# Kernel tuning notes

Measured on AMD Instinct MI355X. Metric: run time of the kernel, lower is better.

The kernel has to match this reference:

```python
import jax, jax.numpy as jnp
import numpy as np

B, H, S, D = 4, 16, 2048, 64

def setup_inputs() -> dict:
    key = jax.random.key(0)
    kq, kk, kv = jax.random.split(key, 3)
    return {
        "input_query": jax.random.normal(kq, (B, H, S, D), dtype=jnp.float32),
        "input_key": jax.random.normal(kk, (B, H, S, D), dtype=jnp.float32),
        "input_value": jax.random.normal(kv, (B, H, S, D), dtype=jnp.float32),
    }

def reference(input_query, input_key, input_value):
    # Unscaled, unmasked attention: softmax(Q K^T) V
    scores = jnp.einsum("bhsd,bhtd->bhst", input_query, input_key)  # [B,H,S,S]
    probs = jax.nn.softmax(scores, axis=-1)
    return jnp.einsum("bhst,bhtd->bhsd", probs, input_value)  # [B,H,S,D]
```

## Files before the change

### kernel.cpp

```cpp
#include <hip/hip_runtime.h>
#include <hip/hip_bf16.h>
#include <stdint.h>

#define SEQ 2048
#define DIM 64
#define NH  64
#define KT  32
#define NT  (SEQ / KT)
#define RAWK_BYTES 8192
#define FRAG_BYTES 12288
#define KF_BYTES   8192

typedef __attribute__((ext_vector_type(8)))  short    bf16x8;
typedef __attribute__((ext_vector_type(8)))  _Float16 f16x8;
typedef __attribute__((ext_vector_type(8)))  float    f32x8;
typedef __attribute__((ext_vector_type(16))) float    f32x16;
typedef unsigned int u32;

#if __has_builtin(__builtin_amdgcn_exp2f)
#define EXP2(x) __builtin_amdgcn_exp2f(x)
#else
#define EXP2(x) exp2f(x)
#endif

__device__ __forceinline__ int phi(int s) {
    int h = (s >> 2) & 1, b = s >> 3, i = s & 3;
    return 8 * h + 4 * b + i + (b >= 2 ? 8 : 0);
}

__global__ __launch_bounds__(768, 6) void attn_fused(
    const float* __restrict__ Q, const float* __restrict__ K,
    const float* __restrict__ V, float* __restrict__ O)
{
    __shared__ __align__(16) char rawK[3][RAWK_BYTES];
    __shared__ __align__(16) char frag[3][FRAG_BYTES];

    const int tid  = threadIdx.x;
    const int wave = tid >> 6, lane = tid & 63;
    const int h = lane >> 5, col = lane & 31;

    const int bid  = blockIdx.x;
    const int head = (bid & 7) * 8 + ((bid >> 3) & 7);
    const size_t base = (size_t)head * SEQ * DIM;

    if (wave < 8) {
        const int qw = (bid >> 6) * 256 + wave * 32;

        f16x8 qf[4];
        {
            const float* qr = Q + base + (size_t)(qw + col) * DIM;
            #pragma unroll
            for (int c = 0; c < 4; ++c)
                #pragma unroll
                for (int j = 0; j < 8; ++j)
                    qf[c][j] = (_Float16)(qr[c * 16 + 8 * h + j] * 1.44269504088896f);
        }

        f32x16 z16;
        #pragma unroll
        for (int r = 0; r < 16; ++r) z16[r] = 0.f;
        f32x16 of[2];
        of[0] = z16; of[1] = z16;
        float l_own = 0.f;

        __builtin_amdgcn_s_barrier();

        int fi = 0;
        for (int kt = 0; kt < NT; ++kt) {
            asm volatile("s_waitcnt lgkmcnt(0)" ::: "memory");
            __builtin_amdgcn_s_barrier();
            __builtin_amdgcn_sched_barrier(0);
            const char* cur = frag[fi];

            f32x16 s = z16;
            __builtin_amdgcn_s_setprio(1);
            #pragma unroll
            for (int c = 0; c < 4; ++c) {
                f16x8 kh = *(const f16x8*)(cur + (c * 2 + 0) * 1024 + lane * 16);
                f16x8 kl = *(const f16x8*)(cur + (c * 2 + 1) * 1024 + lane * 16);
                s = __builtin_amdgcn_mfma_f32_32x32x16_f16(kh, qf[c], s, 0, 0, 0);
                s = __builtin_amdgcn_mfma_f32_32x32x16_f16(kl, qf[c], s, 0, 0, 0);
            }
            __builtin_amdgcn_s_setprio(0);

            bf16x8 pfrag[2];
            {
                float p[16], ls = 0.f;
                #pragma unroll
                for (int r = 0; r < 16; ++r) { p[r] = EXP2(s[r]); ls += p[r]; }
                l_own += ls;
                u32 pk[8];
                #pragma unroll
                for (int m = 0; m < 8; ++m) {
                    __hip_bfloat162 b2 = __float22bfloat162_rn(make_float2(p[2 * m], p[2 * m + 1]));
                    __builtin_memcpy(&pk[m], &b2, 4);
                }
                #pragma unroll
                for (int c = 0; c < 2; ++c) {
                    u32 a0 = pk[4 * c + 0], b0 = pk[4 * c + 2];
                    u32 a1 = pk[4 * c + 1], b1 = pk[4 * c + 3];
                    asm volatile("v_permlane32_swap_b32 %0, %1" : "+v"(a0), "+v"(b0));
                    asm volatile("v_permlane32_swap_b32 %0, %1" : "+v"(a1), "+v"(b1));
                    union { u32 w[4]; bf16x8 v; } fr;
                    fr.w[0] = a0; fr.w[1] = a1; fr.w[2] = b0; fr.w[3] = b1;
                    pfrag[c] = fr.v;
                }
            }

            __builtin_amdgcn_s_setprio(1);
            #pragma unroll
            for (int f = 0; f < 2; ++f)
                #pragma unroll
                for (int c = 0; c < 2; ++c) {
                    bf16x8 vf = *(const bf16x8*)(cur + KF_BYTES + (f * 2 + c) * 1024 + lane * 16);
                    of[f] = __builtin_amdgcn_mfma_f32_32x32x16_bf16(pfrag[c], vf, of[f], 0, 0, 0);
                }
            __builtin_amdgcn_s_setprio(0);

            fi = (fi == 2) ? 0 : fi + 1;
        }

        float* op = O + base;
        {
            float lall = l_own + __shfl_xor(l_own, 32);
            float inv = 1.0f / lall;
            #pragma unroll
            for (int r = 0; r < 16; ++r) {
                int qrow = (r & 3) + 8 * (r >> 2) + 4 * h;
                float iq = __shfl(inv, qrow);
                op[(size_t)(qw + qrow) * DIM + col]      = of[0][r] * iq;
                op[(size_t)(qw + qrow) * DIM + 32 + col] = of[1][r] * iq;
            }
        }
    } else {
        const int pw = wave - 8;
        const float* Kh = K + base;
        const float* Vh = V + base;

        const int fv = pw >> 1, cv = pw & 1;
        int vrow[8];
        #pragma unroll
        for (int j = 0; j < 8; ++j) vrow[j] = phi(16 * cv + 8 * h + j);

        auto stageK = [&](int kt, char* dst) {
            const char* g = (const char*)(Kh + (size_t)kt * (KT * DIM));
            #pragma unroll
            for (int i = 0; i < 2; ++i) {
                const int P  = pw * 128 + i * 64 + lane;
                const int sk = (P & ~15) | ((P & 15) ^ ((P >> 4) & 7));
                char* d = dst + (size_t)(pw * 128 + i * 64) * 16;
                __builtin_amdgcn_global_load_lds(
                    (const __attribute__((address_space(1))) u32*)(g + (size_t)sk * 16),
                    (__attribute__((address_space(3))) u32*)d, 16, 0, 0);
            }
        };
        auto loadV = [&](int kt) -> f32x8 {
            const float* vp = Vh + (size_t)kt * (KT * DIM) + fv * 32 + col;
            f32x8 r;
            #pragma unroll
            for (int j = 0; j < 8; ++j) r[j] = vp[vrow[j] * DIM];
            return r;
        };
        auto convert = [&](const char* rk_, char* fr, f32x8 vv) {
            const int r = phi(col);
            const int kk = 4 * pw + 2 * h;
            const float4* rk4 = (const float4*)rk_;
            float4 a = rk4[r * 16 + ((kk    ) ^ (r & 7))];
            float4 b = rk4[r * 16 + ((kk + 1) ^ (r & 7))];
            float x[8] = {a.x, a.y, a.z, a.w, b.x, b.y, b.z, b.w};
            f16x8 hi, lo;
            #pragma unroll
            for (int j = 0; j < 8; ++j) {
                _Float16 xh = (_Float16)x[j];
                hi[j] = xh;
                lo[j] = (_Float16)(x[j] - (float)xh);
            }
            *(f16x8*)(fr + (pw * 2 + 0) * 1024 + lane * 16) = hi;
            *(f16x8*)(fr + (pw * 2 + 1) * 1024 + lane * 16) = lo;
            union { u32 w[4]; bf16x8 v; } uv;
            #pragma unroll
            for (int j = 0; j < 4; ++j) {
                __hip_bfloat162 b2 = __float22bfloat162_rn(make_float2(vv[2 * j], vv[2 * j + 1]));
                __builtin_memcpy(&uv.w[j], &b2, 4);
            }
            *(bf16x8*)(fr + KF_BYTES + (fv * 2 + cv) * 1024 + lane * 16) = uv.v;
        };

        stageK(0, rawK[0]);
        stageK(1, rawK[1]);
        f32x8 vvA = loadV(0);
        f32x8 vvB = loadV(1);
        asm volatile("s_waitcnt vmcnt(0)" ::: "memory");
        __builtin_amdgcn_s_barrier();
        convert(rawK[0], frag[0], vvA);
        convert(rawK[1], frag[1], vvB);
        stageK(2, rawK[2]);
        vvA = loadV(2);

        int ri = 2, si = 0;
        for (int kt = 0; kt < NT; ++kt) {
            asm volatile("s_waitcnt vmcnt(0) lgkmcnt(0)" ::: "memory");
            __builtin_amdgcn_s_barrier();
            __builtin_amdgcn_sched_barrier(0);

            const bool ld = (kt + 3 < NT);
            if (ld) stageK(kt + 3, rawK[si]);
            f32x8 vnext;
            if (ld) vnext = loadV(kt + 3);
            if (kt + 2 < NT)
                convert(rawK[ri], frag[ri], (kt & 1) ? vvB : vvA);
            if (ld) { if (kt & 1) vvA = vnext; else vvB = vnext; }

            ri = (ri == 2) ? 0 : ri + 1;
            si = (si == 2) ? 0 : si + 1;
        }
    }
}

extern "C" void kernel_launch(void* const* d_in, const int* in_sizes, int n_in,
                              void* d_out, int out_size, void* d_ws, size_t ws_size,
                              hipStream_t stream) {
    const float* Q = (const float*)d_in[0];
    const float* K = (const float*)d_in[1];
    const float* V = (const float*)d_in[2];
    float* Out = (float*)d_out;
    (void)d_ws; (void)ws_size;

    attn_fused<<<dim3(NH * (SEQ / 256)), dim3(768), 0, stream>>>(Q, K, V, Out);
}
```

Before: 229.3 us.

## Process two query tiles per consumer wave and halve block size

Each compute wave now handles 64 query rows (two 32-row tiles) instead of 32. This reuses every K/V fragment read from LDS across two MFMA chains, and halves the number of consumer and producer waves per block (384 threads instead of 768). Producer waves each stage twice as much K and V per tile. The change raises register pressure per wave and lowers the wave count per block, which trades latency hiding for less LDS traffic and fewer barrier participants.

```diff
diff --git a/kernel.cpp b/kernel.cpp
--- a/kernel.cpp
+++ b/kernel.cpp
@@ -28,7 +28,7 @@
     return 8 * h + 4 * b + i + (b >= 2 ? 8 : 0);
 }
 
-__global__ __launch_bounds__(768, 6) void attn_fused(
+__global__ __launch_bounds__(384, 3) void attn_fused(
     const float* __restrict__ Q, const float* __restrict__ K,
     const float* __restrict__ V, float* __restrict__ O)
 {
@@ -43,25 +43,26 @@
     const int head = (bid & 7) * 8 + ((bid >> 3) & 7);
     const size_t base = (size_t)head * SEQ * DIM;
 
-    if (wave < 8) {
-        const int qw = (bid >> 6) * 256 + wave * 32;
-
-        f16x8 qf[4];
-        {
-            const float* qr = Q + base + (size_t)(qw + col) * DIM;
+    if (wave < 4) {
+        const int qw = (bid >> 6) * 256 + wave * 64;
+
+        f16x8 qf[2][4];
+        #pragma unroll
+        for (int qt = 0; qt < 2; ++qt) {
+            const float* qr = Q + base + (size_t)(qw + qt * 32 + col) * DIM;
             #pragma unroll
             for (int c = 0; c < 4; ++c)
                 #pragma unroll
                 for (int j = 0; j < 8; ++j)
-                    qf[c][j] = (_Float16)(qr[c * 16 + 8 * h + j] * 1.44269504088896f);
+                    qf[qt][c][j] = (_Float16)(qr[c * 16 + 8 * h + j] * 1.44269504088896f);
         }
 
         f32x16 z16;
         #pragma unroll
         for (int r = 0; r < 16; ++r) z16[r] = 0.f;
-        f32x16 of[2];
-        of[0] = z16; of[1] = z16;
-        float l_own = 0.f;
+        f32x16 of[2][2];
+        of[0][0] = z16; of[0][1] = z16; of[1][0] = z16; of[1][1] = z16;
+        float l_own[2] = {0.f, 0.f};
 
         __builtin_amdgcn_s_barrier();
 
@@ -72,23 +73,30 @@
             __builtin_amdgcn_sched_barrier(0);
             const char* cur = frag[fi];
 
-            f32x16 s = z16;
+            f32x16 s[2]; s[0] = z16; s[1] = z16;
             __builtin_amdgcn_s_setprio(1);
             #pragma unroll
             for (int c = 0; c < 4; ++c) {
                 f16x8 kh = *(const f16x8*)(cur + (c * 2 + 0) * 1024 + lane * 16);
                 f16x8 kl = *(const f16x8*)(cur + (c * 2 + 1) * 1024 + lane * 16);
-                s = __builtin_amdgcn_mfma_f32_32x32x16_f16(kh, qf[c], s, 0, 0, 0);
-                s = __builtin_amdgcn_mfma_f32_32x32x16_f16(kl, qf[c], s, 0, 0, 0);
+                s[0] = __builtin_amdgcn_mfma_f32_32x32x16_f16(kh, qf[0][c], s[0], 0, 0, 0);
+                s[0] = __builtin_amdgcn_mfma_f32_32x32x16_f16(kl, qf[0][c], s[0], 0, 0, 0);
+                s[1] = __builtin_amdgcn_mfma_f32_32x32x16_f16(kh, qf[1][c], s[1], 0, 0, 0);
+                s[1] = __builtin_amdgcn_mfma_f32_32x32x16_f16(kl, qf[1][c], s[1], 0, 0, 0);
             }
             __builtin_amdgcn_s_setprio(0);
 
-            bf16x8 pfrag[2];
-            {
-                float p[16], ls = 0.f;
-                #pragma unroll
-                for (int r = 0; r < 16; ++r) { p[r] = EXP2(s[r]); ls += p[r]; }
-                l_own += ls;
+            bf16x8 pfrag[2][2];
+            #pragma unroll
+            for (int qt = 0; qt < 2; ++qt) {
+                float p[16];
+                #pragma unroll
+                for (int r = 0; r < 16; ++r) p[r] = EXP2(s[qt][r]);
+                float t0 = (p[0] + p[1]) + (p[2] + p[3]);
+                float t1 = (p[4] + p[5]) + (p[6] + p[7]);
+                float t2 = (p[8] + p[9]) + (p[10] + p[11]);
+                float t3 = (p[12] + p[13]) + (p[14] + p[15]);
+                l_own[qt] += (t0 + t1) + (t2 + t3);
                 u32 pk[8];
                 #pragma unroll
                 for (int m = 0; m < 8; ++m) {
@@ -103,7 +111,7 @@
                     asm volatile("v_permlane32_swap_b32 %0, %1" : "+v"(a1), "+v"(b1));
                     union { u32 w[4]; bf16x8 v; } fr;
                     fr.w[0] = a0; fr.w[1] = a1; fr.w[2] = b0; fr.w[3] = b1;
-                    pfrag[c] = fr.v;
+                    pfrag[qt][c] = fr.v;
                 }
             }
 
@@ -113,7 +121,8 @@
                 #pragma unroll
                 for (int c = 0; c < 2; ++c) {
                     bf16x8 vf = *(const bf16x8*)(cur + KF_BYTES + (f * 2 + c) * 1024 + lane * 16);
-                    of[f] = __builtin_amdgcn_mfma_f32_32x32x16_bf16(pfrag[c], vf, of[f], 0, 0, 0);
+                    of[0][f] = __builtin_amdgcn_mfma_f32_32x32x16_bf16(pfrag[0][c], vf, of[0][f], 0, 0, 0);
+                    of[1][f] = __builtin_amdgcn_mfma_f32_32x32x16_bf16(pfrag[1][c], vf, of[1][f], 0, 0, 0);
                 }
             __builtin_amdgcn_s_setprio(0);
 
@@ -121,81 +130,90 @@
         }
 
         float* op = O + base;
-        {
-            float lall = l_own + __shfl_xor(l_own, 32);
+        #pragma unroll
+        for (int qt = 0; qt < 2; ++qt) {
+            float lall = l_own[qt] + __shfl_xor(l_own[qt], 32);
             float inv = 1.0f / lall;
             #pragma unroll
             for (int r = 0; r < 16; ++r) {
                 int qrow = (r & 3) + 8 * (r >> 2) + 4 * h;
                 float iq = __shfl(inv, qrow);
-                op[(size_t)(qw + qrow) * DIM + col]      = of[0][r] * iq;
-                op[(size_t)(qw + qrow) * DIM + 32 + col] = of[1][r] * iq;
+                op[(size_t)(qw + qt * 32 + qrow) * DIM + col]      = of[qt][0][r] * iq;
+                op[(size_t)(qw + qt * 32 + qrow) * DIM + 32 + col] = of[qt][1][r] * iq;
             }
         }
     } else {
-        const int pw = wave - 8;
+        const int pw = wave - 4;
         const float* Kh = K + base;
         const float* Vh = V + base;
 
-        const int fv = pw >> 1, cv = pw & 1;
-        int vrow[8];
-        #pragma unroll
-        for (int j = 0; j < 8; ++j) vrow[j] = phi(16 * cv + 8 * h + j);
+        const int fv = pw;
+        int vrA[8], vrB[8];
+        #pragma unroll
+        for (int j = 0; j < 8; ++j) { vrA[j] = phi(8 * h + j); vrB[j] = phi(16 + 8 * h + j); }
 
         auto stageK = [&](int kt, char* dst) {
             const char* g = (const char*)(Kh + (size_t)kt * (KT * DIM));
             #pragma unroll
-            for (int i = 0; i < 2; ++i) {
-                const int P  = pw * 128 + i * 64 + lane;
+            for (int i = 0; i < 4; ++i) {
+                const int P  = pw * 256 + i * 64 + lane;
                 const int sk = (P & ~15) | ((P & 15) ^ ((P >> 4) & 7));
-                char* d = dst + (size_t)(pw * 128 + i * 64) * 16;
+                char* d = dst + (size_t)(pw * 256 + i * 64) * 16;
                 __builtin_amdgcn_global_load_lds(
                     (const __attribute__((address_space(1))) u32*)(g + (size_t)sk * 16),
                     (__attribute__((address_space(3))) u32*)d, 16, 0, 0);
             }
         };
-        auto loadV = [&](int kt) -> f32x8 {
+        auto loadV = [&](int kt, f32x8& ra, f32x8& rb) {
             const float* vp = Vh + (size_t)kt * (KT * DIM) + fv * 32 + col;
-            f32x8 r;
-            #pragma unroll
-            for (int j = 0; j < 8; ++j) r[j] = vp[vrow[j] * DIM];
-            return r;
+            #pragma unroll
+            for (int j = 0; j < 8; ++j) ra[j] = vp[vrA[j] * DIM];
+            #pragma unroll
+            for (int j = 0; j < 8; ++j) rb[j] = vp[vrB[j] * DIM];
         };
-        auto convert = [&](const char* rk_, char* fr, f32x8 vv) {
+        auto convert = [&](const char* rk_, char* fr, f32x8 va, f32x8 vb) {
+            const float4* rk4 = (const float4*)rk_;
             const int r = phi(col);
-            const int kk = 4 * pw + 2 * h;
-            const float4* rk4 = (const float4*)rk_;
-            float4 a = rk4[r * 16 + ((kk    ) ^ (r & 7))];
-            float4 b = rk4[r * 16 + ((kk + 1) ^ (r & 7))];
-            float x[8] = {a.x, a.y, a.z, a.w, b.x, b.y, b.z, b.w};
-            f16x8 hi, lo;
-            #pragma unroll
-            for (int j = 0; j < 8; ++j) {
-                _Float16 xh = (_Float16)x[j];
-                hi[j] = xh;
-                lo[j] = (_Float16)(x[j] - (float)xh);
-            }
-            *(f16x8*)(fr + (pw * 2 + 0) * 1024 + lane * 16) = hi;
-            *(f16x8*)(fr + (pw * 2 + 1) * 1024 + lane * 16) = lo;
-            union { u32 w[4]; bf16x8 v; } uv;
+            #pragma unroll
+            for (int cc = 0; cc < 2; ++cc) {
+                const int c = 2 * pw + cc;
+                const int kk = 4 * c + 2 * h;
+                float4 a = rk4[r * 16 + ((kk    ) ^ (r & 7))];
+                float4 b = rk4[r * 16 + ((kk + 1) ^ (r & 7))];
+                float x[8] = {a.x, a.y, a.z, a.w, b.x, b.y, b.z, b.w};
+                f16x8 hi, lo;
+                #pragma unroll
+                for (int j = 0; j < 8; ++j) {
+                    _Float16 xh = (_Float16)x[j];
+                    hi[j] = xh;
+                    lo[j] = (_Float16)(x[j] - (float)xh);
+                }
+                *(f16x8*)(fr + (c * 2 + 0) * 1024 + lane * 16) = hi;
+                *(f16x8*)(fr + (c * 2 + 1) * 1024 + lane * 16) = lo;
+            }
+            union { u32 w[4]; bf16x8 v; } ua, ub;
             #pragma unroll
             for (int j = 0; j < 4; ++j) {
-                __hip_bfloat162 b2 = __float22bfloat162_rn(make_float2(vv[2 * j], vv[2 * j + 1]));
-                __builtin_memcpy(&uv.w[j], &b2, 4);
-            }
-            *(bf16x8*)(fr + KF_BYTES + (fv * 2 + cv) * 1024 + lane * 16) = uv.v;
+                __hip_bfloat162 p2 = __float22bfloat162_rn(make_float2(va[2 * j], va[2 * j + 1]));
+                __builtin_memcpy(&ua.w[j], &p2, 4);
+                __hip_bfloat162 q2 = __float22bfloat162_rn(make_float2(vb[2 * j], vb[2 * j + 1]));
+                __builtin_memcpy(&ub.w[j], &q2, 4);
+            }
+            *(bf16x8*)(fr + KF_BYTES + (fv * 2 + 0) * 1024 + lane * 16) = ua.v;
+            *(bf16x8*)(fr + KF_BYTES + (fv * 2 + 1) * 1024 + lane * 16) = ub.v;
         };
 
         stageK(0, rawK[0]);
         stageK(1, rawK[1]);
-        f32x8 vvA = loadV(0);
-        f32x8 vvB = loadV(1);
+        f32x8 a0, b0, a1, b1;
+        loadV(0, a0, b0);
+        loadV(1, a1, b1);
         asm volatile("s_waitcnt vmcnt(0)" ::: "memory");
         __builtin_amdgcn_s_barrier();
-        convert(rawK[0], frag[0], vvA);
-        convert(rawK[1], frag[1], vvB);
+        convert(rawK[0], frag[0], a0, b0);
+        convert(rawK[1], frag[1], a1, b1);
         stageK(2, rawK[2]);
-        vvA = loadV(2);
+        loadV(2, a0, b0);
 
         int ri = 2, si = 0;
         for (int kt = 0; kt < NT; ++kt) {
@@ -205,11 +223,11 @@
 
             const bool ld = (kt + 3 < NT);
             if (ld) stageK(kt + 3, rawK[si]);
-            f32x8 vnext;
-            if (ld) vnext = loadV(kt + 3);
+            f32x8 na, nb;
+            if (ld) loadV(kt + 3, na, nb);
             if (kt + 2 < NT)
-                convert(rawK[ri], frag[ri], (kt & 1) ? vvB : vvA);
-            if (ld) { if (kt & 1) vvA = vnext; else vvB = vnext; }
+                convert(rawK[ri], frag[ri], (kt & 1) ? a1 : a0, (kt & 1) ? b1 : b0);
+            if (ld) { if (kt & 1) { a0 = na; b0 = nb; } else { a1 = na; b1 = nb; } }
 
             ri = (ri == 2) ? 0 : ri + 1;
             si = (si == 2) ? 0 : si + 1;
@@ -226,5 +244,5 @@
     float* Out = (float*)d_out;
     (void)d_ws; (void)ws_size;
 
-    attn_fused<<<dim3(NH * (SEQ / 256)), dim3(768), 0, stream>>>(Q, K, V, Out);
+    attn_fused<<<dim3(NH * (SEQ / 256)), dim3(384), 0, stream>>>(Q, K, V, Out);
 }
```

New measurement: 278.4 us. 21.4% more time.

## Process two key tiles per barrier and load K directly to registers

Applied to the files above, without the earlier changes.

The consumer loop now handles two 32-key tiles per barrier, cutting the number of block-wide barriers in half. Producer waves now read K straight from global memory into registers, dropping the raw-K LDS staging buffers and the global_load_lds path. The fragment buffer ring grows from three to four slots. Producer loads are now issued and waited on within the same iteration instead of being prefetched a step ahead, so global-memory latency may be less hidden. The row-sum is also rewritten as a tree reduction.

```diff
diff --git a/kernel.cpp b/kernel.cpp
--- a/kernel.cpp
+++ b/kernel.cpp
@@ -7,7 +7,7 @@
 #define NH  64
 #define KT  32
 #define NT  (SEQ / KT)
-#define RAWK_BYTES 8192
+#define NW  (NT / 2)
 #define FRAG_BYTES 12288
 #define KF_BYTES   8192
 
@@ -32,8 +32,7 @@
     const float* __restrict__ Q, const float* __restrict__ K,
     const float* __restrict__ V, float* __restrict__ O)
 {
-    __shared__ __align__(16) char rawK[3][RAWK_BYTES];
-    __shared__ __align__(16) char frag[3][FRAG_BYTES];
+    __shared__ __align__(16) char frag[4][FRAG_BYTES];
 
     const int tid  = threadIdx.x;
     const int wave = tid >> 6, lane = tid & 63;
@@ -65,59 +64,64 @@
 
         __builtin_amdgcn_s_barrier();
 
-        int fi = 0;
-        for (int kt = 0; kt < NT; ++kt) {
+        for (int w = 0; w < NW; ++w) {
             asm volatile("s_waitcnt lgkmcnt(0)" ::: "memory");
             __builtin_amdgcn_s_barrier();
             __builtin_amdgcn_sched_barrier(0);
-            const char* cur = frag[fi];
-
-            f32x16 s = z16;
-            __builtin_amdgcn_s_setprio(1);
-            #pragma unroll
-            for (int c = 0; c < 4; ++c) {
-                f16x8 kh = *(const f16x8*)(cur + (c * 2 + 0) * 1024 + lane * 16);
-                f16x8 kl = *(const f16x8*)(cur + (c * 2 + 1) * 1024 + lane * 16);
-                s = __builtin_amdgcn_mfma_f32_32x32x16_f16(kh, qf[c], s, 0, 0, 0);
-                s = __builtin_amdgcn_mfma_f32_32x32x16_f16(kl, qf[c], s, 0, 0, 0);
-            }
-            __builtin_amdgcn_s_setprio(0);
-
-            bf16x8 pfrag[2];
-            {
-                float p[16], ls = 0.f;
+
+            #pragma unroll
+            for (int tt = 0; tt < 2; ++tt) {
+                const char* cur = frag[(2 * w + tt) & 3];
+
+                f32x16 s = z16;
+                __builtin_amdgcn_s_setprio(1);
                 #pragma unroll
-                for (int r = 0; r < 16; ++r) { p[r] = EXP2(s[r]); ls += p[r]; }
-                l_own += ls;
-                u32 pk[8];
+                for (int c = 0; c < 4; ++c) {
+                    f16x8 kh = *(const f16x8*)(cur + (c * 2 + 0) * 1024 + lane * 16);
+                    f16x8 kl = *(const f16x8*)(cur + (c * 2 + 1) * 1024 + lane * 16);
+                    s = __builtin_amdgcn_mfma_f32_32x32x16_f16(kh, qf[c], s, 0, 0, 0);
+                    s = __builtin_amdgcn_mfma_f32_32x32x16_f16(kl, qf[c], s, 0, 0, 0);
+                }
+                __builtin_amdgcn_s_setprio(0);
+
+                bf16x8 pfrag[2];
+                {
+                    float p[16];
+                    #pragma unroll
+                    for (int r = 0; r < 16; ++r) p[r] = EXP2(s[r]);
+                    float t0 = (p[0] + p[1]) + (p[2] + p[3]);
+                    float t1 = (p[4] + p[5]) + (p[6] + p[7]);
+                    float t2 = (p[8] + p[9]) + (p[10] + p[11]);
+                    float t3 = (p[12] + p[13]) + (p[14] + p[15]);
+                    l_own += (t0 + t1) + (t2 + t3);
+                    u32 pk[8];
+                    #pragma unroll
+                    for (int m = 0; m < 8; ++m) {
+                        __hip_bfloat162 b2 = __float22bfloat162_rn(make_float2(p[2 * m], p[2 * m + 1]));
+                        __builtin_memcpy(&pk[m], &b2, 4);
+                    }
+                    #pragma unroll
+                    for (int c = 0; c < 2; ++c) {
+                        u32 a0 = pk[4 * c + 0], b0 = pk[4 * c + 2];
+                        u32 a1 = pk[4 * c + 1], b1 = pk[4 * c + 3];
+                        asm volatile("v_permlane32_swap_b32 %0, %1" : "+v"(a0), "+v"(b0));
+                        asm volatile("v_permlane32_swap_b32 %0, %1" : "+v"(a1), "+v"(b1));
+                        union { u32 w[4]; bf16x8 v; } fr;
+                        fr.w[0] = a0; fr.w[1] = a1; fr.w[2] = b0; fr.w[3] = b1;
+                        pfrag[c] = fr.v;
+                    }
+                }
+
+                __builtin_amdgcn_s_setprio(1);
                 #pragma unroll
-                for (int m = 0; m < 8; ++m) {
-                    __hip_bfloat162 b2 = __float22bfloat162_rn(make_float2(p[2 * m], p[2 * m + 1]));
-                    __builtin_memcpy(&pk[m], &b2, 4);
-                }
-                #pragma unroll
-                for (int c = 0; c < 2; ++c) {
-                    u32 a0 = pk[4 * c + 0], b0 = pk[4 * c + 2];
-                    u32 a1 = pk[4 * c + 1], b1 = pk[4 * c + 3];
-                    asm volatile("v_permlane32_swap_b32 %0, %1" : "+v"(a0), "+v"(b0));
-                    asm volatile("v_permlane32_swap_b32 %0, %1" : "+v"(a1), "+v"(b1));
-                    union { u32 w[4]; bf16x8 v; } fr;
-                    fr.w[0] = a0; fr.w[1] = a1; fr.w[2] = b0; fr.w[3] = b1;
-                    pfrag[c] = fr.v;
-                }
-            }
-
-            __builtin_amdgcn_s_setprio(1);
-            #pragma unroll
-            for (int f = 0; f < 2; ++f)
-                #pragma unroll
-                for (int c = 0; c < 2; ++c) {
-                    bf16x8 vf = *(const bf16x8*)(cur + KF_BYTES + (f * 2 + c) * 1024 + lane * 16);
-                    of[f] = __builtin_amdgcn_mfma_f32_32x32x16_bf16(pfrag[c], vf, of[f], 0, 0, 0);
-                }
-            __builtin_amdgcn_s_setprio(0);
-
-            fi = (fi == 2) ? 0 : fi + 1;
+                for (int f = 0; f < 2; ++f)
+                    #pragma unroll
+                    for (int c = 0; c < 2; ++c) {
+                        bf16x8 vf = *(const bf16x8*)(cur + KF_BYTES + (f * 2 + c) * 1024 + lane * 16);
+                        of[f] = __builtin_amdgcn_mfma_f32_32x32x16_bf16(pfrag[c], vf, of[f], 0, 0, 0);
+                    }
+                __builtin_amdgcn_s_setprio(0);
+            }
         }
 
         float* op = O + base;
@@ -137,36 +141,25 @@
         const float* Kh = K + base;
         const float* Vh = V + base;
 
+        const float* kbase = Kh + (size_t)phi(col) * DIM + 16 * pw + 8 * h;
         const int fv = pw >> 1, cv = pw & 1;
         int vrow[8];
         #pragma unroll
         for (int j = 0; j < 8; ++j) vrow[j] = phi(16 * cv + 8 * h + j);
 
-        auto stageK = [&](int kt, char* dst) {
-            const char* g = (const char*)(Kh + (size_t)kt * (KT * DIM));
-            #pragma unroll
-            for (int i = 0; i < 2; ++i) {
-                const int P  = pw * 128 + i * 64 + lane;
-                const int sk = (P & ~15) | ((P & 15) ^ ((P >> 4) & 7));
-                char* d = dst + (size_t)(pw * 128 + i * 64) * 16;
-                __builtin_amdgcn_global_load_lds(
-                    (const __attribute__((address_space(1))) u32*)(g + (size_t)sk * 16),
-                    (__attribute__((address_space(3))) u32*)d, 16, 0, 0);
-            }
+        auto loadK = [&](int t, float4& a, float4& b) {
+            const float* kp = kbase + (size_t)t * (KT * DIM);
+            a = *(const float4*)kp;
+            b = *(const float4*)(kp + 4);
         };
-        auto loadV = [&](int kt) -> f32x8 {
-            const float* vp = Vh + (size_t)kt * (KT * DIM) + fv * 32 + col;
+        auto loadV = [&](int t) -> f32x8 {
+            const float* vp = Vh + (size_t)t * (KT * DIM) + fv * 32 + col;
             f32x8 r;
             #pragma unroll
             for (int j = 0; j < 8; ++j) r[j] = vp[vrow[j] * DIM];
             return r;
         };
-        auto convert = [&](const char* rk_, char* fr, f32x8 vv) {
-            const int r = phi(col);
-            const int kk = 4 * pw + 2 * h;
-            const float4* rk4 = (const float4*)rk_;
-            float4 a = rk4[r * 16 + ((kk    ) ^ (r & 7))];
-            float4 b = rk4[r * 16 + ((kk + 1) ^ (r & 7))];
+        auto convert = [&](char* fr, float4 a, float4 b, f32x8 vv) {
             float x[8] = {a.x, a.y, a.z, a.w, b.x, b.y, b.z, b.w};
             f16x8 hi, lo;
             #pragma unroll
@@ -186,33 +179,30 @@
             *(bf16x8*)(fr + KF_BYTES + (fv * 2 + cv) * 1024 + lane * 16) = uv.v;
         };
 
-        stageK(0, rawK[0]);
-        stageK(1, rawK[1]);
-        f32x8 vvA = loadV(0);
-        f32x8 vvB = loadV(1);
+        float4 ka0, kb0, ka1, kb1;
+        loadK(0, ka0, kb0);
+        loadK(1, ka1, kb1);
+        f32x8 vv0 = loadV(0);
+        f32x8 vv1 = loadV(1);
         asm volatile("s_waitcnt vmcnt(0)" ::: "memory");
+        convert(frag[0], ka0, kb0, vv0);
+        convert(frag[1], ka1, kb1, vv1);
+        asm volatile("s_waitcnt lgkmcnt(0)" ::: "memory");
         __builtin_amdgcn_s_barrier();
-        convert(rawK[0], frag[0], vvA);
-        convert(rawK[1], frag[1], vvB);
-        stageK(2, rawK[2]);
-        vvA = loadV(2);
-
-        int ri = 2, si = 0;
-        for (int kt = 0; kt < NT; ++kt) {
-            asm volatile("s_waitcnt vmcnt(0) lgkmcnt(0)" ::: "memory");
+
+        for (int w = 0; w < NW; ++w) {
             __builtin_amdgcn_s_barrier();
             __builtin_amdgcn_sched_barrier(0);
-
-            const bool ld = (kt + 3 < NT);
-            if (ld) stageK(kt + 3, rawK[si]);
-            f32x8 vnext;
-            if (ld) vnext = loadV(kt + 3);
-            if (kt + 2 < NT)
-                convert(rawK[ri], frag[ri], (kt & 1) ? vvB : vvA);
-            if (ld) { if (kt & 1) vvA = vnext; else vvB = vnext; }
-
-            ri = (ri == 2) ? 0 : ri + 1;
-            si = (si == 2) ? 0 : si + 1;
+            if (2 * w + 2 < NT) {
+                loadK(2 * w + 2, ka0, kb0);
+                loadK(2 * w + 3, ka1, kb1);
+                vv0 = loadV(2 * w + 2);
+                vv1 = loadV(2 * w + 3);
+                asm volatile("s_waitcnt vmcnt(0)" ::: "memory");
+                convert(frag[(2 * w + 2) & 3], ka0, kb0, vv0);
+                convert(frag[(2 * w + 3) & 3], ka1, kb1, vv1);
+            }
+            asm volatile("s_waitcnt lgkmcnt(0)" ::: "memory");
         }
     }
 }
```

Result: faster. 223.9 us (-2.4%).
